# Performance work log

Hardware: AMD Instinct MI355X
Metric: run time of the kernel (lower is better)

## Reference

```python
import jax, jax.numpy as jnp
import numpy as np

N = 50000
E = 800000
D = 96


def setup_inputs() -> dict:
    key = jax.random.key(0)
    ks = jax.random.split(key, 9)
    x = jax.random.normal(ks[0], (N, D), dtype=jnp.float32)
    edge_index = jax.random.randint(ks[1], (2, E), 0, N, dtype=jnp.int64)
    s = 1.0 / np.sqrt(D)
    # PyG GraphConv: lin_rel (with bias) on aggregated neighbors, lin_root (no bias) on self.
    W1_rel = jax.random.uniform(ks[2], (D, D), jnp.float32, -s, s)
    b1_rel = jax.random.uniform(ks[3], (D,), jnp.float32, -s, s)
    W1_root = jax.random.uniform(ks[4], (D, D), jnp.float32, -s, s)
    W2_rel = jax.random.uniform(ks[5], (D, D), jnp.float32, -s, s)
    b2_rel = jax.random.uniform(ks[6], (D,), jnp.float32, -s, s)
    W2_root = jax.random.uniform(ks[7], (D, D), jnp.float32, -s, s)
    return {
        "x": x, "edge_index": edge_index,
        "W1_rel": W1_rel, "b1_rel": b1_rel, "W1_root": W1_root,
        "W2_rel": W2_rel, "b2_rel": b2_rel, "W2_root": W2_root,
    }


def _graph_conv(x, src, dst, W_rel, b_rel, W_root):
    # gather source features, sum-scatter to destinations (PyG aggr='add')
    agg = jax.ops.segment_sum(x[src], dst, num_segments=N)  # [N, D]
    return agg @ W_rel + b_rel + x @ W_root


def reference(x, edge_index, W1_rel, b1_rel, W1_root, W2_rel, b2_rel, W2_root):
    src, dst = edge_index[0], edge_index[1]
    h = jax.nn.relu(_graph_conv(x, src, dst, W1_rel, b1_rel, W1_root))
    out = _graph_conv(h, src, dst, W2_rel, b2_rel, W2_root)
    return out
```

## Files before the change

kernel.cpp:

```cpp
#include <hip/hip_runtime.h>
#include <hip/hip_bf16.h>

#define DD 96
#define CB_BITS 7
#define CB_SIZE 128
#define CB_MAXBINS 512
#define CBE 2048
#define BIN_CAP 4096

typedef __attribute__((ext_vector_type(8))) short short8;
typedef __attribute__((ext_vector_type(4))) float floatx4;

__device__ __forceinline__ int load_idx(const void* eidx, int isI64, int pos) {
    return isI64 ? (int)((const long long*)eidx)[pos] : ((const int*)eidx)[pos];
}

__device__ __forceinline__ unsigned int b16(float f) {
    unsigned int u = __float_as_uint(f);
    return (u + 0x7fffu + ((u >> 16) & 1u)) >> 16;
}
__device__ __forceinline__ unsigned int pack2(float lo, float hi) {
    return b16(lo) | (b16(hi) << 16);
}

__global__ __launch_bounds__(256) void prep_kernel(
    const float* __restrict__ x,
    const float* __restrict__ W1_rel, const float* __restrict__ W1_root,
    const float* __restrict__ W2_rel, const float* __restrict__ W2_root,
    const unsigned long long* __restrict__ idx64,
    int* __restrict__ flag, int* __restrict__ binCursor,
    unsigned short* __restrict__ xb,
    uint4* __restrict__ wpack1, uint4* __restrict__ wpack2,
    long long nelem, unsigned long long nmax, int nbins) {
    const int b = blockIdx.x;
    const int tid = threadIdx.x;
    if (b == 0) {
        __shared__ int bad;
        if (tid == 0) bad = 0;
        __syncthreads();
        unsigned long long v = idx64[tid];
        if (v >= nmax) bad = 1;
        __syncthreads();
        if (tid == 0) *flag = bad ? 0 : 1;
        for (int i = tid; i < nbins; i += 256) binCursor[i] = i * BIN_CAP;
        return;
    }
    if (b <= 18) {
        int t = (b - 1) * 256 + tid;
        int layer = t / 2304;
        int tt = t - layer * 2304;
        const float* Wr = layer ? W2_rel : W1_rel;
        const float* Wo = layer ? W2_root : W1_root;
        uint4* wp = layer ? wpack2 : wpack1;
        int f = tt >> 6, lane = tt & 63;
        int kt = f / 6, nt = f % 6;
        int n = nt * 16 + (lane & 15);
        int kbase = kt * 32 + (lane >> 4) * 8;
        float v[8];
        #pragma unroll
        for (int j = 0; j < 8; ++j) {
            int k = kbase + j;
            v[j] = (k < DD) ? Wr[(size_t)k * DD + n]
                            : Wo[(size_t)(k - DD) * DD + n];
        }
        uint4 o;
        o.x = pack2(v[0], v[1]); o.y = pack2(v[2], v[3]);
        o.z = pack2(v[4], v[5]); o.w = pack2(v[6], v[7]);
        wp[tt] = o;
        return;
    }
    long long i = ((long long)(b - 19) * 256 + tid) * 8;
    if (i + 8 > nelem) return;
    float4 f0 = ((const float4*)(x + i))[0];
    float4 f1 = ((const float4*)(x + i))[1];
    uint4 o;
    o.x = pack2(f0.x, f0.y); o.y = pack2(f0.z, f0.w);
    o.z = pack2(f1.x, f1.y); o.w = pack2(f1.z, f1.w);
    *((uint4*)(xb + i)) = o;
}

__global__ __launch_bounds__(256) void coarse_bin_kernel(
    const void* __restrict__ eidx, const int* __restrict__ flag,
    int* __restrict__ binCursor, uint2* __restrict__ estage,
    int E, int n, int nbins) {
    __shared__ int cnt[CB_MAXBINS];
    __shared__ int pref[CB_MAXBINS];
    __shared__ int cur[CB_MAXBINS];
    __shared__ int gbase[CB_MAXBINS];
    __shared__ uint2 ebuf[CBE];
    __shared__ int tot_sh;
    const int tid = threadIdx.x;
    for (int i = tid; i < CB_MAXBINS; i += 256) cnt[i] = 0;
    __syncthreads();
    const int base = blockIdx.x * CBE;
    const int isI64 = *flag;
    for (int k = tid; k < CBE; k += 256) {
        int e = base + k;
        if (e < E) {
            int s = load_idx(eidx, isI64, e);
            int d = load_idx(eidx, isI64, E + e);
            if ((unsigned)s < (unsigned)n && (unsigned)d < (unsigned)n)
                atomicAdd(&cnt[d >> CB_BITS], 1);
        }
    }
    __syncthreads();
    {
        int a0 = cnt[2 * tid], a1 = cnt[2 * tid + 1];
        int ps = a0 + a1;
        gbase[tid] = ps;
        __syncthreads();
        int v = ps;
        for (int off = 1; off < 256; off <<= 1) {
            int o = (tid >= off) ? gbase[tid - off] : 0;
            __syncthreads();
            v += o;
            gbase[tid] = v;
            __syncthreads();
        }
        int ex = v - ps;
        pref[2 * tid] = ex;      pref[2 * tid + 1] = ex + a0;
        cur[2 * tid]  = ex;      cur[2 * tid + 1]  = ex + a0;
        if (tid == 255) tot_sh = v;
    }
    __syncthreads();
    const int tot = tot_sh;
    for (int k = tid; k < CBE; k += 256) {
        int e = base + k;
        if (e < E) {
            int s = load_idx(eidx, isI64, e);
            int d = load_idx(eidx, isI64, E + e);
            if ((unsigned)s < (unsigned)n && (unsigned)d < (unsigned)n) {
                int r = atomicAdd(&cur[d >> CB_BITS], 1);
                ebuf[r] = make_uint2((unsigned)s, (unsigned)d);
            }
        }
    }
    __syncthreads();
    for (int i = tid; i < nbins; i += 256) {
        int c = cnt[i];
        gbase[i] = c ? atomicAdd(&binCursor[i], c) : 0;
    }
    __syncthreads();
    for (int k = tid; k < tot; k += 256) {
        uint2 e = ebuf[k];
        int bin = (int)(e.y >> CB_BITS);
        int g = gbase[bin] + (k - pref[bin]);
        if (g < (bin + 1) * BIN_CAP) estage[g] = e;
    }
}

__device__ __forceinline__ void acc8(float* a, uint4 w) {
    a[0] += __uint_as_float(w.x << 16); a[1] += __uint_as_float(w.x & 0xffff0000u);
    a[2] += __uint_as_float(w.y << 16); a[3] += __uint_as_float(w.y & 0xffff0000u);
    a[4] += __uint_as_float(w.z << 16); a[5] += __uint_as_float(w.z & 0xffff0000u);
    a[6] += __uint_as_float(w.w << 16); a[7] += __uint_as_float(w.w & 0xffff0000u);
}

__global__ __launch_bounds__(256) void gather_bin_kernel(
    const uint2* __restrict__ estage, const int* __restrict__ binCursor,
    const unsigned short* __restrict__ feat, unsigned short* __restrict__ aggb,
    int n) {
    __shared__ int cnt[CB_SIZE];
    __shared__ int stl[CB_SIZE];
    __shared__ int cur[CB_SIZE];
    __shared__ int pref[CB_SIZE];
    __shared__ int ssrc_l[BIN_CAP];
    const int b = blockIdx.x;
    const int tid = threadIdx.x;
    const uint2* ebin = estage + (size_t)b * BIN_CAP;
    int tot = binCursor[b] - b * BIN_CAP;
    tot = (tot < 0) ? 0 : (tot > BIN_CAP ? BIN_CAP : tot);
    if (tid < CB_SIZE) cnt[tid] = 0;
    __syncthreads();
    for (int k = tid; k < tot; k += 256)
        atomicAdd(&cnt[ebin[k].y & (CB_SIZE - 1)], 1);
    __syncthreads();
    {
        int v = (tid < CB_SIZE) ? cnt[tid] : 0;
        if (tid < CB_SIZE) pref[tid] = v;
        __syncthreads();
        for (int off = 1; off < CB_SIZE; off <<= 1) {
            int o = (tid < CB_SIZE && tid >= off) ? pref[tid - off] : 0;
            __syncthreads();
            if (tid < CB_SIZE) { v += o; pref[tid] = v; }
            __syncthreads();
        }
        if (tid < CB_SIZE) {
            int st = v - cnt[tid];
            stl[tid] = st;
            cur[tid] = st;
        }
    }
    __syncthreads();
    for (int k = tid; k < tot; k += 256) {
        uint2 e = ebin[k];
        int pos = atomicAdd(&cur[e.y & (CB_SIZE - 1)], 1);
        ssrc_l[pos] = (int)e.x;
    }
    __syncthreads();
    #pragma unroll
    for (int it = 0; it < 6; ++it) {
        int p = it * 256 + tid;
        int nl = p / 12, c = p % 12;
        int node = (b << CB_BITS) + nl;
        if (node >= n) continue;
        int st = stl[nl], en = st + cnt[nl];
        float accA[8] = {0,0,0,0,0,0,0,0};
        float accB[8] = {0,0,0,0,0,0,0,0};
        int j = st;
        for (; j + 4 <= en; j += 4) {
            int s0 = ssrc_l[j + 0], s1 = ssrc_l[j + 1];
            int s2 = ssrc_l[j + 2], s3 = ssrc_l[j + 3];
            uint4 w0 = ((const uint4*)(feat + (size_t)s0 * DD))[c];
            uint4 w1 = ((const uint4*)(feat + (size_t)s1 * DD))[c];
            uint4 w2 = ((const uint4*)(feat + (size_t)s2 * DD))[c];
            uint4 w3 = ((const uint4*)(feat + (size_t)s3 * DD))[c];
            acc8(accA, w0); acc8(accB, w1); acc8(accA, w2); acc8(accB, w3);
        }
        for (; j < en; ++j) {
            uint4 w = ((const uint4*)(feat + (size_t)ssrc_l[j] * DD))[c];
            acc8(accA, w);
        }
        uint4 o;
        o.x = pack2(accA[0] + accB[0], accA[1] + accB[1]);
        o.y = pack2(accA[2] + accB[2], accA[3] + accB[3]);
        o.z = pack2(accA[4] + accB[4], accA[5] + accB[5]);
        o.w = pack2(accA[6] + accB[6], accA[7] + accB[7]);
        *((uint4*)(aggb + (size_t)node * DD + (size_t)c * 8)) = o;
    }
}

__global__ __launch_bounds__(256, 3) void linear_mfma_kernel(
    const unsigned short* __restrict__ Ab, const unsigned short* __restrict__ Xb,
    const uint4* __restrict__ wpack, const float* __restrict__ bias,
    float* __restrict__ outf, unsigned short* __restrict__ outb,
    int n, int do_relu) {
    const int lane = threadIdx.x & 63;
    const int w = threadIdx.x >> 6;
    const int p = w >> 1;
    const int sub = w & 1;
    const int m16 = lane & 15;
    const int quad = lane >> 4;
    const int base = blockIdx.x * 64;

    short8 bfrag[6][3];
    #pragma unroll
    for (int kt = 0; kt < 6; ++kt)
        #pragma unroll
        for (int ntl = 0; ntl < 3; ++ntl) {
            uint4 u = wpack[(kt * 6 + (p * 3 + ntl)) * 64 + lane];
            bfrag[kt][ntl] = *(short8*)&u;
        }

    floatx4 acc[2][3];
    #pragma unroll
    for (int mi = 0; mi < 2; ++mi)
        #pragma unroll
        for (int ntl = 0; ntl < 3; ++ntl)
            acc[mi][ntl] = (floatx4){0.f, 0.f, 0.f, 0.f};

    #pragma unroll
    for (int kt = 0; kt < 6; ++kt) {
        const unsigned short* src = (kt < 3) ? Ab : Xb;
        const int koff = (kt < 3 ? kt : kt - 3) * 32 + quad * 8;
        short8 afrag[2];
        #pragma unroll
        for (int mi = 0; mi < 2; ++mi) {
            int row = base + (sub + mi * 2) * 16 + m16;
            int r = (row < n) ? row : 0;
            afrag[mi] = *(const short8*)(src + (size_t)r * DD + koff);
        }
        #pragma unroll
        for (int ntl = 0; ntl < 3; ++ntl) {
            acc[0][ntl] = __builtin_amdgcn_mfma_f32_16x16x32_bf16(
                afrag[0], bfrag[kt][ntl], acc[0][ntl], 0, 0, 0);
            acc[1][ntl] = __builtin_amdgcn_mfma_f32_16x16x32_bf16(
                afrag[1], bfrag[kt][ntl], acc[1][ntl], 0, 0, 0);
        }
    }

    #pragma unroll
    for (int ntl = 0; ntl < 3; ++ntl) {
        const int col = (p * 3 + ntl) * 16 + m16;
        const float bv = bias[col];
        #pragma unroll
        for (int mi = 0; mi < 2; ++mi) {
            #pragma unroll
            for (int reg = 0; reg < 4; ++reg) {
                int row = base + (sub + mi * 2) * 16 + quad * 4 + reg;
                if (row < n) {
                    float v = acc[mi][ntl][reg] + bv;
                    if (do_relu) v = fmaxf(v, 0.f);
                    if (outf) outf[(size_t)row * DD + col] = v;
                    if (outb) outb[(size_t)row * DD + col] =
                        (unsigned short)b16(v);
                }
            }
        }
    }
}

__global__ void detect_idx_kernel(const unsigned long long* __restrict__ idx,
                                  int* __restrict__ flag,
                                  unsigned long long nmax) {
    __shared__ int bad;
    if (threadIdx.x == 0) bad = 0;
    __syncthreads();
    unsigned long long v = idx[threadIdx.x];
    if (v >= nmax) bad = 1;
    __syncthreads();
    if (threadIdx.x == 0) *flag = bad ? 0 : 1;
}

__global__ __launch_bounds__(256) void scatter_add_kernel(
    const float* __restrict__ feat, const void* __restrict__ eidx,
    const int* __restrict__ flag, float* __restrict__ agg,
    int E, int n) {
    long long t = (long long)blockIdx.x * 256 + threadIdx.x;
    if (t >= (long long)E * 24) return;
    int e = (int)(t / 24);
    int c = (int)(t % 24);
    int isI64 = *flag;
    int s = load_idx(eidx, isI64, e);
    int d = load_idx(eidx, isI64, E + e);
    if ((unsigned)s >= (unsigned)n || (unsigned)d >= (unsigned)n) return;
    const float4 v = ((const float4*)(feat + (size_t)s * DD))[c];
    float* o = agg + (size_t)d * DD + (size_t)c * 4;
    atomicAdd(o + 0, v.x);
    atomicAdd(o + 1, v.y);
    atomicAdd(o + 2, v.z);
    atomicAdd(o + 3, v.w);
}

__global__ __launch_bounds__(256, 4) void linear64_kernel(
    const float* __restrict__ A, const float* __restrict__ X,
    const float* __restrict__ Wrel, const float* __restrict__ bias,
    const float* __restrict__ Wroot, float* __restrict__ out,
    int n, int do_relu) {
    __shared__ float wlds[DD * DD];
    const int lane = threadIdx.x & 63;
    const int q = threadIdx.x >> 6;
    const int j0 = q * 24;
    const int node = blockIdx.x * 64 + lane;
    const bool act = (node < n);
    const int r = act ? node : 0;
    float acc[24];
    {
        const float4* bq = (const float4*)(bias + j0);
        #pragma unroll
        for (int jj = 0; jj < 6; ++jj) {
            float4 b = bq[jj];
            acc[jj*4+0] = b.x; acc[jj*4+1] = b.y;
            acc[jj*4+2] = b.z; acc[jj*4+3] = b.w;
        }
    }
    const float* srcs[2] = {A, X};
    const float* mats[2] = {Wrel, Wroot};
    for (int phase = 0; phase < 2; ++phase) {
        {
            const float4* wg = (const float4*)mats[phase];
            float4* wl = (float4*)wlds;
            #pragma unroll
            for (int i = 0; i < 9; ++i)
                wl[threadIdx.x + i * 256] = wg[threadIdx.x + i * 256];
        }
        __syncthreads();
        const float* row = srcs[phase] + (size_t)r * DD;
        for (int kk = 0; kk < DD; kk += 4) {
            float4 a4 = *(const float4*)(row + kk);
            const float av[4] = {a4.x, a4.y, a4.z, a4.w};
            #pragma unroll
            for (int u = 0; u < 4; ++u) {
                const float4* wrow = (const float4*)(&wlds[(kk + u) * DD + j0]);
                const float ka = av[u];
                #pragma unroll
                for (int jj = 0; jj < 6; ++jj) {
                    float4 ww = wrow[jj];
                    acc[jj*4+0] = fmaf(ka, ww.x, acc[jj*4+0]);
                    acc[jj*4+1] = fmaf(ka, ww.y, acc[jj*4+1]);
                    acc[jj*4+2] = fmaf(ka, ww.z, acc[jj*4+2]);
                    acc[jj*4+3] = fmaf(ka, ww.w, acc[jj*4+3]);
                }
            }
        }
        __syncthreads();
    }
    if (act) {
        float4* o = (float4*)(out + (size_t)node * DD + j0);
        #pragma unroll
        for (int jj = 0; jj < 6; ++jj) {
            float4 v = make_float4(acc[jj*4+0], acc[jj*4+1],
                                   acc[jj*4+2], acc[jj*4+3]);
            if (do_relu) {
                v.x = fmaxf(v.x, 0.f); v.y = fmaxf(v.y, 0.f);
                v.z = fmaxf(v.z, 0.f); v.w = fmaxf(v.w, 0.f);
            }
            o[jj] = v;
        }
    }
}

__global__ __launch_bounds__(256) void linear_kernel(
    const float* __restrict__ A, const float* __restrict__ X,
    const float* __restrict__ Wrel, const float* __restrict__ bias,
    const float* __restrict__ Wroot, float* __restrict__ out,
    int n, int do_relu) {
    __shared__ float wlds[DD * DD];
    const int lane = threadIdx.x & 63;
    const int q = threadIdx.x >> 6;
    const int j0 = q * 24;
    const int m0 = blockIdx.x * 128 + lane;
    const int m1 = m0 + 64;
    const bool act0 = (m0 < n), act1 = (m1 < n);
    const int r0 = act0 ? m0 : 0;
    const int r1 = act1 ? m1 : 0;
    float acc0[24], acc1[24];
    {
        const float4* bq = (const float4*)(bias + j0);
        #pragma unroll
        for (int jj = 0; jj < 6; ++jj) {
            float4 b = bq[jj];
            acc0[jj*4+0] = b.x; acc0[jj*4+1] = b.y;
            acc0[jj*4+2] = b.z; acc0[jj*4+3] = b.w;
            acc1[jj*4+0] = b.x; acc1[jj*4+1] = b.y;
            acc1[jj*4+2] = b.z; acc1[jj*4+3] = b.w;
        }
    }
    const float* srcs[2] = {A, X};
    const float* mats[2] = {Wrel, Wroot};
    for (int phase = 0; phase < 2; ++phase) {
        {
            const float4* wg = (const float4*)mats[phase];
            float4* wl = (float4*)wlds;
            #pragma unroll
            for (int i = 0; i < 9; ++i)
                wl[threadIdx.x + i * 256] = wg[threadIdx.x + i * 256];
        }
        __syncthreads();
        const float* row0 = srcs[phase] + (size_t)r0 * DD;
        const float* row1 = srcs[phase] + (size_t)r1 * DD;
        for (int kk = 0; kk < DD; kk += 4) {
            float4 a0 = *(const float4*)(row0 + kk);
            float4 a1 = *(const float4*)(row1 + kk);
            const float av0[4] = {a0.x, a0.y, a0.z, a0.w};
            const float av1[4] = {a1.x, a1.y, a1.z, a1.w};
            #pragma unroll
            for (int u = 0; u < 4; ++u) {
                const float4* wrow = (const float4*)(&wlds[(kk + u) * DD + j0]);
                const float k0 = av0[u], k1 = av1[u];
                #pragma unroll
                for (int jj = 0; jj < 6; ++jj) {
                    float4 ww = wrow[jj];
                    acc0[jj*4+0] = fmaf(k0, ww.x, acc0[jj*4+0]);
                    acc0[jj*4+1] = fmaf(k0, ww.y, acc0[jj*4+1]);
                    acc0[jj*4+2] = fmaf(k0, ww.z, acc0[jj*4+2]);
                    acc0[jj*4+3] = fmaf(k0, ww.w, acc0[jj*4+3]);
                    acc1[jj*4+0] = fmaf(k1, ww.x, acc1[jj*4+0]);
                    acc1[jj*4+1] = fmaf(k1, ww.y, acc1[jj*4+1]);
                    acc1[jj*4+2] = fmaf(k1, ww.z, acc1[jj*4+2]);
                    acc1[jj*4+3] = fmaf(k1, ww.w, acc1[jj*4+3]);
                }
            }
        }
        __syncthreads();
    }
    if (act0) {
        float4* o = (float4*)(out + (size_t)m0 * DD + j0);
        #pragma unroll
        for (int jj = 0; jj < 6; ++jj) {
            float4 v = make_float4(acc0[jj*4+0], acc0[jj*4+1],
                                   acc0[jj*4+2], acc0[jj*4+3]);
            if (do_relu) {
                v.x = fmaxf(v.x, 0.f); v.y = fmaxf(v.y, 0.f);
                v.z = fmaxf(v.z, 0.f); v.w = fmaxf(v.w, 0.f);
            }
            o[jj] = v;
        }
    }
    if (act1) {
        float4* o = (float4*)(out + (size_t)m1 * DD + j0);
        #pragma unroll
        for (int jj = 0; jj < 6; ++jj) {
            float4 v = make_float4(acc1[jj*4+0], acc1[jj*4+1],
                                   acc1[jj*4+2], acc1[jj*4+3]);
            if (do_relu) {
                v.x = fmaxf(v.x, 0.f); v.y = fmaxf(v.y, 0.f);
                v.z = fmaxf(v.z, 0.f); v.w = fmaxf(v.w, 0.f);
            }
            o[jj] = v;
        }
    }
}

extern "C" void kernel_launch(void* const* d_in, const int* in_sizes, int n_in,
                              void* d_out, int out_size, void* d_ws, size_t ws_size,
                              hipStream_t stream) {
    const float* x      = (const float*)d_in[0];
    const void*  eidx   = d_in[1];
    const float* W1_rel = (const float*)d_in[2];
    const float* b1     = (const float*)d_in[3];
    const float* W1_root= (const float*)d_in[4];
    const float* W2_rel = (const float*)d_in[5];
    const float* b2     = (const float*)d_in[6];
    const float* W2_root= (const float*)d_in[7];
    float* out = (float*)d_out;

    const int N = in_sizes[0] / DD;
    const int E = in_sizes[1] / 2;
    const int nbins = (N + CB_SIZE - 1) >> CB_BITS;
    const long long nelem = (long long)N * DD;
    char* base = (char*)d_ws;

    size_t off = 0;
    auto alloc = [&](size_t bytes) {
        size_t o = off; off = (off + bytes + 255) & ~(size_t)255; return base + o; };
    int*   flag      = (int*)  alloc(256);
    int*   binCursor = (int*)  alloc((size_t)(CB_MAXBINS + 1) * 4);
    uint2* estage    = (uint2*)alloc((size_t)nbins * BIN_CAP * 8);
    unsigned short* xb   = (unsigned short*)alloc((size_t)nelem * 2);
    unsigned short* hb   = (unsigned short*)alloc((size_t)nelem * 2);
    unsigned short* aggb = (unsigned short*)alloc((size_t)nelem * 2);
    uint4* wpack1    = (uint4*)alloc(36 * 64 * 16);
    uint4* wpack2    = (uint4*)alloc(36 * 64 * 16);
    const bool mfma_ok = (off <= ws_size) && (nbins <= CB_MAXBINS) &&
                         (nbins > 0) && (3LL * (E / nbins) <= 2LL * BIN_CAP);

    size_t offB = 512;
    auto allocB = [&](size_t bytes) {
        size_t o = offB; offB = (offB + bytes + 255) & ~(size_t)255; return base + o; };
    float* agg = (float*)allocB((size_t)nelem * 4);
    const bool fb_ok = (offB <= ws_size);

    if (mfma_ok) {
        const int conv_blocks = (int)((nelem / 8 + 255) / 256);
        const int mfma_blocks = (N + 63) / 64;
        prep_kernel<<<19 + conv_blocks, 256, 0, stream>>>(
            x, W1_rel, W1_root, W2_rel, W2_root,
            (const unsigned long long*)eidx, flag, binCursor,
            xb, wpack1, wpack2, nelem, (unsigned long long)N, nbins);
        coarse_bin_kernel<<<(E + CBE - 1) / CBE, 256, 0, stream>>>(
            eidx, flag, binCursor, estage, E, N, nbins);
        gather_bin_kernel<<<nbins, 256, 0, stream>>>(
            estage, binCursor, xb, aggb, N);
        linear_mfma_kernel<<<mfma_blocks, 256, 0, stream>>>(
            aggb, xb, wpack1, b1, (float*)nullptr, hb, N, 1);
        gather_bin_kernel<<<nbins, 256, 0, stream>>>(
            estage, binCursor, hb, aggb, N);
        linear_mfma_kernel<<<mfma_blocks, 256, 0, stream>>>(
            aggb, hb, wpack2, b2, out, (unsigned short*)nullptr, N, 0);
    } else if (fb_ok) {
        const int scatter_blocks = (int)(((long long)E * 24 + 255) / 256);
        detect_idx_kernel<<<1, 256, 0, stream>>>(
            (const unsigned long long*)eidx, flag, (unsigned long long)N);
        hipMemsetAsync(agg, 0, (size_t)nelem * 4, stream);
        scatter_add_kernel<<<scatter_blocks, 256, 0, stream>>>(x, eidx, flag, agg, E, N);
        linear64_kernel<<<(N + 63) / 64, 256, 0, stream>>>(
            agg, x, W1_rel, b1, W1_root, out, N, 1);
        hipMemsetAsync(agg, 0, (size_t)nelem * 4, stream);
        scatter_add_kernel<<<scatter_blocks, 256, 0, stream>>>(out, eidx, flag, agg, E, N);
        linear_kernel<<<(N + 127) / 128, 256, 0, stream>>>(
            agg, out, W2_rel, b2, W2_root, out, N, 0);
    }
}
```

Before: 191.3 us.

## Fuse neighbor gather with MFMA linear into one per-bin layer kernel

```diff
diff --git a/kernel.cpp b/kernel.cpp
--- a/kernel.cpp
+++ b/kernel.cpp
@@ -7,6 +7,7 @@
 #define CB_MAXBINS 512
 #define CBE 2048
 #define BIN_CAP 4096
+#define AGG_STRIDE 104
 
 typedef __attribute__((ext_vector_type(8))) short short8;
 typedef __attribute__((ext_vector_type(4))) float floatx4;
@@ -94,13 +95,18 @@
     __syncthreads();
     const int base = blockIdx.x * CBE;
     const int isI64 = *flag;
-    for (int k = tid; k < CBE; k += 256) {
-        int e = base + k;
+    int sr[8], dr[8];
+    #pragma unroll
+    for (int i = 0; i < 8; ++i) {
+        int e = base + tid + i * 256;
+        sr[i] = -1; dr[i] = -1;
         if (e < E) {
             int s = load_idx(eidx, isI64, e);
             int d = load_idx(eidx, isI64, E + e);
-            if ((unsigned)s < (unsigned)n && (unsigned)d < (unsigned)n)
+            if ((unsigned)s < (unsigned)n && (unsigned)d < (unsigned)n) {
+                sr[i] = s; dr[i] = d;
                 atomicAdd(&cnt[d >> CB_BITS], 1);
+            }
         }
     }
     __syncthreads();
@@ -124,15 +130,11 @@
     }
     __syncthreads();
     const int tot = tot_sh;
-    for (int k = tid; k < CBE; k += 256) {
-        int e = base + k;
-        if (e < E) {
-            int s = load_idx(eidx, isI64, e);
-            int d = load_idx(eidx, isI64, E + e);
-            if ((unsigned)s < (unsigned)n && (unsigned)d < (unsigned)n) {
-                int r = atomicAdd(&cur[d >> CB_BITS], 1);
-                ebuf[r] = make_uint2((unsigned)s, (unsigned)d);
-            }
+    #pragma unroll
+    for (int i = 0; i < 8; ++i) {
+        if (dr[i] >= 0) {
+            int r = atomicAdd(&cur[dr[i] >> CB_BITS], 1);
+            ebuf[r] = make_uint2((unsigned)sr[i], (unsigned)dr[i]);
         }
     }
     __syncthreads();
@@ -156,15 +158,17 @@
     a[6] += __uint_as_float(w.w << 16); a[7] += __uint_as_float(w.w & 0xffff0000u);
 }
 
-__global__ __launch_bounds__(256) void gather_bin_kernel(
+__global__ __launch_bounds__(512) void layer_kernel(
     const uint2* __restrict__ estage, const int* __restrict__ binCursor,
-    const unsigned short* __restrict__ feat, unsigned short* __restrict__ aggb,
-    int n) {
+    const unsigned short* __restrict__ feat, const uint4* __restrict__ wpack,
+    const float* __restrict__ bias, float* __restrict__ outf,
+    unsigned short* __restrict__ outb, int n, int do_relu) {
     __shared__ int cnt[CB_SIZE];
     __shared__ int stl[CB_SIZE];
     __shared__ int cur[CB_SIZE];
     __shared__ int pref[CB_SIZE];
     __shared__ int ssrc_l[BIN_CAP];
+    __shared__ unsigned short agg_l[CB_SIZE * AGG_STRIDE];
     const int b = blockIdx.x;
     const int tid = threadIdx.x;
     const uint2* ebin = estage + (size_t)b * BIN_CAP;
@@ -172,7 +176,7 @@
     tot = (tot < 0) ? 0 : (tot > BIN_CAP ? BIN_CAP : tot);
     if (tid < CB_SIZE) cnt[tid] = 0;
     __syncthreads();
-    for (int k = tid; k < tot; k += 256)
+    for (int k = tid; k < tot; k += 512)
         atomicAdd(&cnt[ebin[k].y & (CB_SIZE - 1)], 1);
     __syncthreads();
     {
@@ -192,108 +196,112 @@
         }
     }
     __syncthreads();
-    for (int k = tid; k < tot; k += 256) {
+    for (int k = tid; k < tot; k += 512) {
         uint2 e = ebin[k];
         int pos = atomicAdd(&cur[e.y & (CB_SIZE - 1)], 1);
         ssrc_l[pos] = (int)e.x;
     }
     __syncthreads();
     #pragma unroll
-    for (int it = 0; it < 6; ++it) {
-        int p = it * 256 + tid;
+    for (int it = 0; it < 3; ++it) {
+        int p = it * 512 + tid;
         int nl = p / 12, c = p % 12;
         int node = (b << CB_BITS) + nl;
-        if (node >= n) continue;
-        int st = stl[nl], en = st + cnt[nl];
         float accA[8] = {0,0,0,0,0,0,0,0};
         float accB[8] = {0,0,0,0,0,0,0,0};
-        int j = st;
-        for (; j + 4 <= en; j += 4) {
-            int s0 = ssrc_l[j + 0], s1 = ssrc_l[j + 1];
-            int s2 = ssrc_l[j + 2], s3 = ssrc_l[j + 3];
-            uint4 w0 = ((const uint4*)(feat + (size_t)s0 * DD))[c];
-            uint4 w1 = ((const uint4*)(feat + (size_t)s1 * DD))[c];
-            uint4 w2 = ((const uint4*)(feat + (size_t)s2 * DD))[c];
-            uint4 w3 = ((const uint4*)(feat + (size_t)s3 * DD))[c];
-            acc8(accA, w0); acc8(accB, w1); acc8(accA, w2); acc8(accB, w3);
-        }
-        for (; j < en; ++j) {
-            uint4 w = ((const uint4*)(feat + (size_t)ssrc_l[j] * DD))[c];
-            acc8(accA, w);
+        if (node < n) {
+            int st = stl[nl], en = st + cnt[nl];
+            int j = st;
+            for (; j + 4 <= en; j += 4) {
+                int s0 = ssrc_l[j + 0], s1 = ssrc_l[j + 1];
+                int s2 = ssrc_l[j + 2], s3 = ssrc_l[j + 3];
+                uint4 w0 = ((const uint4*)(feat + (size_t)s0 * DD))[c];
+                uint4 w1 = ((const uint4*)(feat + (size_t)s1 * DD))[c];
+                uint4 w2 = ((const uint4*)(feat + (size_t)s2 * DD))[c];
+                uint4 w3 = ((const uint4*)(feat + (size_t)s3 * DD))[c];
+                acc8(accA, w0); acc8(accB, w1); acc8(accA, w2); acc8(accB, w3);
+            }
+            for (; j < en; ++j) {
+                uint4 w = ((const uint4*)(feat + (size_t)ssrc_l[j] * DD))[c];
+                acc8(accA, w);
+            }
         }
         uint4 o;
         o.x = pack2(accA[0] + accB[0], accA[1] + accB[1]);
         o.y = pack2(accA[2] + accB[2], accA[3] + accB[3]);
         o.z = pack2(accA[4] + accB[4], accA[5] + accB[5]);
         o.w = pack2(accA[6] + accB[6], accA[7] + accB[7]);
-        *((uint4*)(aggb + (size_t)node * DD + (size_t)c * 8)) = o;
-    }
-}
-
-__global__ __launch_bounds__(256, 3) void linear_mfma_kernel(
-    const unsigned short* __restrict__ Ab, const unsigned short* __restrict__ Xb,
-    const uint4* __restrict__ wpack, const float* __restrict__ bias,
-    float* __restrict__ outf, unsigned short* __restrict__ outb,
-    int n, int do_relu) {
-    const int lane = threadIdx.x & 63;
-    const int w = threadIdx.x >> 6;
-    const int p = w >> 1;
-    const int sub = w & 1;
-    const int m16 = lane & 15;
-    const int quad = lane >> 4;
-    const int base = blockIdx.x * 64;
-
-    short8 bfrag[6][3];
-    #pragma unroll
-    for (int kt = 0; kt < 6; ++kt)
+        *((uint4*)&agg_l[nl * AGG_STRIDE + c * 8]) = o;
+    }
+    __syncthreads();
+    {
+        const int lane = tid & 63;
+        const int w = tid >> 6;
+        const int p = w >> 2;
+        const int mt0 = w & 3;
+        const int m16 = lane & 15;
+        const int quad = lane >> 4;
+        const int rowbase = b << CB_BITS;
+
+        short8 bfrag[6][3];
+        #pragma unroll
+        for (int kt = 0; kt < 6; ++kt)
+            #pragma unroll
+            for (int ntl = 0; ntl < 3; ++ntl) {
+                uint4 u = wpack[(kt * 6 + (p * 3 + ntl)) * 64 + lane];
+                bfrag[kt][ntl] = *(short8*)&u;
+            }
+
+        floatx4 acc[2][3];
+        #pragma unroll
+        for (int mi = 0; mi < 2; ++mi)
+            #pragma unroll
+            for (int ntl = 0; ntl < 3; ++ntl)
+                acc[mi][ntl] = (floatx4){0.f, 0.f, 0.f, 0.f};
+
+        #pragma unroll
+        for (int kt = 0; kt < 6; ++kt) {
+            short8 afrag[2];
+            #pragma unroll
+            for (int mi = 0; mi < 2; ++mi) {
+                const int mt = mt0 + mi * 4;
+                const int mrow = mt * 16 + m16;
+                if (kt < 3) {
+                    afrag[mi] = *(const short8*)
+                        &agg_l[mrow * AGG_STRIDE + kt * 32 + quad * 8];
+                } else {
+                    int row = rowbase + mrow;
+                    int r = (row < n) ? row : 0;
+                    afrag[mi] = *(const short8*)
+                        (feat + (size_t)r * DD + (kt - 3) * 32 + quad * 8);
+                }
+            }
+            #pragma unroll
+            for (int ntl = 0; ntl < 3; ++ntl) {
+                acc[0][ntl] = __builtin_amdgcn_mfma_f32_16x16x32_bf16(
+                    afrag[0], bfrag[kt][ntl], acc[0][ntl], 0, 0, 0);
+                acc[1][ntl] = __builtin_amdgcn_mfma_f32_16x16x32_bf16(
+                    afrag[1], bfrag[kt][ntl], acc[1][ntl], 0, 0, 0);
+            }
+        }
+
         #pragma unroll
         for (int ntl = 0; ntl < 3; ++ntl) {
-            uint4 u = wpack[(kt * 6 + (p * 3 + ntl)) * 64 + lane];
-            bfrag[kt][ntl] = *(short8*)&u;
-        }
-
-    floatx4 acc[2][3];
-    #pragma unroll
-    for (int mi = 0; mi < 2; ++mi)
-        #pragma unroll
-        for (int ntl = 0; ntl < 3; ++ntl)
-            acc[mi][ntl] = (floatx4){0.f, 0.f, 0.f, 0.f};
-
-    #pragma unroll
-    for (int kt = 0; kt < 6; ++kt) {
-        const unsigned short* src = (kt < 3) ? Ab : Xb;
-        const int koff = (kt < 3 ? kt : kt - 3) * 32 + quad * 8;
-        short8 afrag[2];
-        #pragma unroll
-        for (int mi = 0; mi < 2; ++mi) {
-            int row = base + (sub + mi * 2) * 16 + m16;
-            int r = (row < n) ? row : 0;
-            afrag[mi] = *(const short8*)(src + (size_t)r * DD + koff);
-        }
-        #pragma unroll
-        for (int ntl = 0; ntl < 3; ++ntl) {
-            acc[0][ntl] = __builtin_amdgcn_mfma_f32_16x16x32_bf16(
-                afrag[0], bfrag[kt][ntl], acc[0][ntl], 0, 0, 0);
-            acc[1][ntl] = __builtin_amdgcn_mfma_f32_16x16x32_bf16(
-                afrag[1], bfrag[kt][ntl], acc[1][ntl], 0, 0, 0);
-        }
-    }
-
-    #pragma unroll
-    for (int ntl = 0; ntl < 3; ++ntl) {
-        const int col = (p * 3 + ntl) * 16 + m16;
-        const float bv = bias[col];
-        #pragma unroll
-        for (int mi = 0; mi < 2; ++mi) {
-            #pragma unroll
-            for (int reg = 0; reg < 4; ++reg) {
-                int row = base + (sub + mi * 2) * 16 + quad * 4 + reg;
-                if (row < n) {
-                    float v = acc[mi][ntl][reg] + bv;
-                    if (do_relu) v = fmaxf(v, 0.f);
-                    if (outf) outf[(size_t)row * DD + col] = v;
-                    if (outb) outb[(size_t)row * DD + col] =
-                        (unsigned short)b16(v);
+            const int col = (p * 3 + ntl) * 16 + m16;
+            const float bv = bias[col];
+            #pragma unroll
+            for (int mi = 0; mi < 2; ++mi) {
+                const int mt = mt0 + mi * 4;
+                #pragma unroll
+                for (int reg = 0; reg < 4; ++reg) {
+                    int row = rowbase + mt * 16 + quad * 4 + reg;
+                    if (row < n) {
+                        float v = acc[mi][ntl][reg] + bv;
+                        if (do_relu) v = fmaxf(v, 0.f);
+                        if (outf) outf[(size_t)row * DD + col] = v;
+                        if (outb) outb[(size_t)row * DD + col] =
+                            (unsigned short)b16(v);
+                    }
                 }
             }
         }
@@ -519,7 +527,6 @@
     uint2* estage    = (uint2*)alloc((size_t)nbins * BIN_CAP * 8);
     unsigned short* xb   = (unsigned short*)alloc((size_t)nelem * 2);
     unsigned short* hb   = (unsigned short*)alloc((size_t)nelem * 2);
-    unsigned short* aggb = (unsigned short*)alloc((size_t)nelem * 2);
     uint4* wpack1    = (uint4*)alloc(36 * 64 * 16);
     uint4* wpack2    = (uint4*)alloc(36 * 64 * 16);
     const bool mfma_ok = (off <= ws_size) && (nbins <= CB_MAXBINS) &&
@@ -533,21 +540,18 @@
 
     if (mfma_ok) {
         const int conv_blocks = (int)((nelem / 8 + 255) / 256);
-        const int mfma_blocks = (N + 63) / 64;
         prep_kernel<<<19 + conv_blocks, 256, 0, stream>>>(
             x, W1_rel, W1_root, W2_rel, W2_root,
             (const unsigned long long*)eidx, flag, binCursor,
             xb, wpack1, wpack2, nelem, (unsigned long long)N, nbins);
         coarse_bin_kernel<<<(E + CBE - 1) / CBE, 256, 0, stream>>>(
             eidx, flag, binCursor, estage, E, N, nbins);
-        gather_bin_kernel<<<nbins, 256, 0, stream>>>(
-            estage, binCursor, xb, aggb, N);
-        linear_mfma_kernel<<<mfma_blocks, 256, 0, stream>>>(
-            aggb, xb, wpack1, b1, (float*)nullptr, hb, N, 1);
-        gather_bin_kernel<<<nbins, 256, 0, stream>>>(
-            estage, binCursor, hb, aggb, N);
-        linear_mfma_kernel<<<mfma_blocks, 256, 0, stream>>>(
-            aggb, hb, wpack2, b2, out, (unsigned short*)nullptr, N, 0);
+        layer_kernel<<<nbins, 512, 0, stream>>>(
+            estage, binCursor, xb, wpack1, b1,
+            (float*)nullptr, hb, N, 1);
+        layer_kernel<<<nbins, 512, 0, stream>>>(
+            estage, binCursor, hb, wpack2, b2,
+            out, (unsigned short*)nullptr, N, 0);
     } else if (fb_ok) {
         const int scatter_blocks = (int)(((long long)E * 24 + 255) / 256);
         detect_idx_kernel<<<1, 256, 0, stream>>>(
```

Result: faster. 167.6 us (-12.4%).
